# Optimization experiments

Hardware: AMD Instinct MI355X
Metric: run time of the kernel (lower is better)

Reference implementation:

```python
import jax, jax.numpy as jnp
import numpy as np

D_MODEL = 1024
NUM_HEADS = 16
HEAD_DIM = D_MODEL // NUM_HEADS          # 64
ROT_W = HEAD_DIM // 2                    # partial_factor=(0.0, 0.5) -> rotary on first half
MAX_LEN = 2048
BASE = 10000.0


def _rope_tables(max_len):
    # theta over even dims of ROT_W, each repeated twice (interleaved pairs): [t0,t0,t1,t1,...]
    theta = 1.0 / (BASE ** (np.arange(0, ROT_W, 2, dtype=np.float32) / ROT_W))  # [ROT_W/2]
    m = np.arange(max_len, dtype=np.float32)[:, None] * theta[None, :]          # [max_len, ROT_W/2]
    m = np.repeat(m, 2, axis=-1)                                                # [max_len, ROT_W]
    return jnp.asarray(np.cos(m)), jnp.asarray(np.sin(m))


def _rotate(x):
    # interleaved pairs (x0, x1) -> (-x1, x0)
    xr = x.reshape(x.shape[:-1] + (-1, 2))
    rot = jnp.stack([-xr[..., 1], xr[..., 0]], axis=-1)
    return rot.reshape(x.shape)


def setup_inputs() -> dict:
    key = jax.random.key(0)
    k1, k2, k3, k4 = jax.random.split(key, 4)
    B, L, H, E = 2, 2048, NUM_HEADS, HEAD_DIM
    return {
        "queries": jax.random.normal(k1, (B, L, H, E), jnp.float32),
        "keys": jax.random.normal(k2, (B, L, H, E), jnp.float32),
        "values": jax.random.normal(k3, (B, L, H, E), jnp.float32),
        "bias_weight": jax.random.normal(k4, (2, H), jnp.float32) * 0.02,  # BinaryAttentionBias embedding
        "n_vars": 32,
        "n_tokens": 64,
    }


def reference(queries, keys, values, bias_weight, n_vars, n_tokens):
    B, L, H, E = queries.shape
    q = queries.transpose(0, 2, 1, 3)  # [B,H,L,E]
    k = keys.transpose(0, 2, 1, 3)     # [B,H,L,E]

    # --- partial rotary projection (shared for q and k), seq_id = arange(L) ---
    cos, sin = _rope_tables(MAX_LEN)
    seq = jnp.arange(n_vars * n_tokens)
    c = cos[seq][None, None]  # [1,1,L,ROT_W]
    s = sin[seq][None, None]

    def rope(x):
        xr = x[..., :ROT_W]
        return jnp.concatenate([c * xr + s * _rotate(xr), x[..., ROT_W:]], axis=-1)

    q = rope(q)
    k = rope(k)

    scale = 1.0 / np.sqrt(E).astype(np.float32)

    # --- binary attention bias: per-head scalar by variable-id equality ---
    var_id = jnp.repeat(jnp.arange(n_vars), n_tokens)          # [L]
    same_var = var_id[:, None] == var_id[None, :]              # [L,L]
    bias = jnp.where(same_var[None, :, :],
                     bias_weight[1][:, None, None],
                     bias_weight[0][:, None, None])            # [H,L,L]

    # --- TimerMultivariateMask: causal in time, full across variables ---
    time_id = seq % n_tokens
    causal_bad = time_id[None, :] > time_id[:, None]           # key time > query time
    attn_mask = jnp.where(causal_bad[None], -jnp.inf, bias)    # [H,L,L]

    scores = jnp.einsum('bhle,bhse->bhls', q, k)               # [B,H,L,L]
    A = jax.nn.softmax(scale * scores + attn_mask[None], axis=-1)
    V = jnp.einsum('bhls,bshd->blhd', A, values)               # [B,L,H,E]
    return V
```

## Files before the change

kernel.cpp:

```cpp
#include <hip/hip_runtime.h>

typedef unsigned short u16;
typedef unsigned int u32;

typedef __attribute__((ext_vector_type(8))) __bf16 bf16x8;
typedef __attribute__((ext_vector_type(4))) float floatx4;

#define B_ 2
#define L_ 2048
#define H_ 16
#define E_ 64
#define QK_ELEMS (B_ * H_ * L_ * E_)
#define WS_OFF 128

static __device__ __forceinline__ float bf2f(u16 v) {
  u32 u = ((u32)v) << 16;
  return __builtin_bit_cast(float, u);
}
static __device__ __forceinline__ u16 f2bf(float x) {
  u32 u = __builtin_bit_cast(u32, x);
  u32 r = (u + 0x7FFFu + ((u >> 16) & 1u)) >> 16;
  return (u16)r;
}

static __device__ __forceinline__ u32 cvtpk_bf16(float lo, float hi) {
  u32 r;
  asm("v_cvt_pk_bf16_f32 %0, %1, %2" : "=v"(r) : "v"(lo), "v"(hi));
  return r;
}

static __device__ __forceinline__ float exp2_fast(float x) {
  float r;
  asm("v_exp_f32 %0, %1" : "=v"(r) : "v"(x));
  return r;
}

static __device__ __forceinline__ void sincos_fast(float a, float* s, float* c) {
  const float INV2PI = 0.15915494309189535f;
  float r = a * INV2PI;
  r = r - floorf(r);
  float ss, cc;
  asm("v_sin_f32 %0, %1" : "=v"(ss) : "v"(r));
  asm("v_cos_f32 %0, %1" : "=v"(cc) : "v"(r));
  *s = ss;
  *c = cc;
}

static __device__ __forceinline__ bool detect_f32_spread(const void* q, u32 blk) {
  const u32* q32 = (const u32*)q;
  u32 off = ((blk & 1023u) << 6) + (threadIdx.x & 63);
  u32 w0 = q32[off];
  u32 w1 = q32[off + 65536];
  int big = ((((w0 >> 7) & 0xFF) > 180) | (((w0 >> 23) & 0xFF) > 180) |
             (((w1 >> 7) & 0xFF) > 180) | (((w1 >> 23) & 0xFF) > 180));
  return __ballot(big) != 0ULL;
}

__global__ void detect_dtype(const u16* __restrict__ q, int* __restrict__ flag) {
  int lane = threadIdx.x;
  int big = 0;
#pragma unroll
  for (int i = 0; i < 16; ++i) {
    u16 v = q[lane * 16 + i];
    int e = (v >> 7) & 0xFF;
    big |= (e > 180);
  }
  unsigned long long b = __ballot(big);
  if (lane == 0) *flag = (b != 0ULL) ? 1 : 0;
}

static __device__ __forceinline__ bf16x8 ld8(const void* base, size_t off, bool f32) {
  if (f32) {
    const float* p = (const float*)base + off;
    float4 a = *(const float4*)p;
    float4 bb = *(const float4*)(p + 4);
    uint4 o;
    o.x = (u32)f2bf(a.x) | ((u32)f2bf(a.y) << 16);
    o.y = (u32)f2bf(a.z) | ((u32)f2bf(a.w) << 16);
    o.z = (u32)f2bf(bb.x) | ((u32)f2bf(bb.y) << 16);
    o.w = (u32)f2bf(bb.z) | ((u32)f2bf(bb.w) << 16);
    return __builtin_bit_cast(bf16x8, o);
  }
  return *(const bf16x8*)((const u16*)base + off);
}

static __device__ __forceinline__ bf16x8 rope_frag(bf16x8 x, float pos, int quad) {
  uint4 u = __builtin_bit_cast(uint4, x);
  float v0 = bf2f((u16)u.x), v1 = bf2f((u16)(u.x >> 16));
  float v2 = bf2f((u16)u.y), v3 = bf2f((u16)(u.y >> 16));
  float v4 = bf2f((u16)u.z), v5 = bf2f((u16)(u.z >> 16));
  float v6 = bf2f((u16)u.w), v7 = bf2f((u16)(u.w >> 16));
  const float LB = 0.83048202372184058696f;
  float jb = (float)(quad * 4);
  float a0 = pos * exp2_fast(-jb * LB);
  float a1 = pos * exp2_fast(-(jb + 1.f) * LB);
  float a2 = pos * exp2_fast(-(jb + 2.f) * LB);
  float a3 = pos * exp2_fast(-(jb + 3.f) * LB);
  float s0, c0, s1, c1, s2, c2, s3, c3;
  sincos_fast(a0, &s0, &c0);
  sincos_fast(a1, &s1, &c1);
  sincos_fast(a2, &s2, &c2);
  sincos_fast(a3, &s3, &c3);
  uint4 o;
  o.x = (u32)f2bf(c0 * v0 - s0 * v1) | ((u32)f2bf(c0 * v1 + s0 * v0) << 16);
  o.y = (u32)f2bf(c1 * v2 - s1 * v3) | ((u32)f2bf(c1 * v3 + s1 * v2) << 16);
  o.z = (u32)f2bf(c2 * v4 - s2 * v5) | ((u32)f2bf(c2 * v5 + s2 * v4) << 16);
  o.w = (u32)f2bf(c3 * v6 - s3 * v7) | ((u32)f2bf(c3 * v7 + s3 * v6) << 16);
  return __builtin_bit_cast(bf16x8, o);
}

__global__ __launch_bounds__(256) void prep_kv(
    const void* __restrict__ Q, const void* __restrict__ K, const void* __restrict__ V,
    u16* __restrict__ Kr, u16* __restrict__ VT) {
  __shared__ u16 tile[64][65];
  const int t = threadIdx.x;
  const bool f32 = detect_f32_spread(Q, blockIdx.x);

  if (blockIdx.x < (B_ * L_)) {
    const int bl = blockIdx.x;
    const int b = bl >> 11, l = bl & (L_ - 1);
    const int h = t >> 4, d = (t & 15) << 2;
    size_t in_off = (((size_t)(b * L_ + l) * H_ + h) * E_) + d;
    size_t out_off = (((size_t)(b * H_ + h) * L_ + l) * E_) + d;
    float k0, k1, k2, k3;
    if (f32) {
      float4 kv = *(const float4*)((const float*)K + in_off);
      k0 = kv.x; k1 = kv.y; k2 = kv.z; k3 = kv.w;
    } else {
      uint2 kv = *(const uint2*)((const u16*)K + in_off);
      k0 = bf2f((u16)kv.x); k1 = bf2f((u16)(kv.x >> 16));
      k2 = bf2f((u16)kv.y); k3 = bf2f((u16)(kv.y >> 16));
    }
    if (d < 32) {
      int j0 = d >> 1;
      const float LB = 0.83048202372184058696f;
      float a0 = (float)l * exp2_fast(-(float)j0 * LB);
      float a1 = (float)l * exp2_fast(-(float)(j0 + 1) * LB);
      float s0, c0, s1, c1;
      sincos_fast(a0, &s0, &c0);
      sincos_fast(a1, &s1, &c1);
      float r;
      r = c0 * k0 - s0 * k1; k1 = c0 * k1 + s0 * k0; k0 = r;
      r = c1 * k2 - s1 * k3; k3 = c1 * k3 + s1 * k2; k2 = r;
    }
    uint2 ko;
    ko.x = (u32)f2bf(k0) | ((u32)f2bf(k1) << 16);
    ko.y = (u32)f2bf(k2) | ((u32)f2bf(k3) << 16);
    *(uint2*)(Kr + out_off) = ko;
  } else {
    const int blk = blockIdx.x - (B_ * L_);
    const int bh = blk & 31, lt = blk >> 5;
    const int b = bh >> 4, h = bh & 15;
    const int l0 = lt << 6;
#pragma unroll
    for (int it = 0; it < 2; ++it) {
      int ll = (t >> 3) + (it << 5);
      int dc = (t & 7) << 3;
      size_t off = (((size_t)(b * L_ + l0 + ll) * H_ + h) * E_) + dc;
      bf16x8 x8 = ld8(V, off, f32);
      uint4 x = __builtin_bit_cast(uint4, x8);
      tile[ll][dc + 0] = (u16)x.x; tile[ll][dc + 1] = (u16)(x.x >> 16);
      tile[ll][dc + 2] = (u16)x.y; tile[ll][dc + 3] = (u16)(x.y >> 16);
      tile[ll][dc + 4] = (u16)x.z; tile[ll][dc + 5] = (u16)(x.z >> 16);
      tile[ll][dc + 6] = (u16)x.w; tile[ll][dc + 7] = (u16)(x.w >> 16);
    }
    __syncthreads();
    int e = t >> 2, lg = (t & 3) << 4;
    u32 pk[8];
#pragma unroll
    for (int i = 0; i < 8; ++i)
      pk[i] = (u32)tile[lg + 2 * i][e] | ((u32)tile[lg + 2 * i + 1][e] << 16);
    u16* dst = VT + (((size_t)(bh * 32 + lt)) << 12) + e * 64 + lg;
    uint4 o0; o0.x = pk[0]; o0.y = pk[1]; o0.z = pk[2]; o0.w = pk[3];
    uint4 o1; o1.x = pk[4]; o1.y = pk[5]; o1.z = pk[6]; o1.w = pk[7];
    *(uint4*)dst = o0;
    *(uint4*)(dst + 8) = o1;
  }
}

#if __has_builtin(__builtin_amdgcn_global_load_lds)
#define HAS_GLL 1
static __device__ __forceinline__ void gll16(const void* g, void* l) {
  __builtin_amdgcn_global_load_lds(
      (const __attribute__((address_space(1))) u32*)g,
      (__attribute__((address_space(3))) u32*)l, 16, 0, 0);
}
#else
#define HAS_GLL 0
#endif

__global__ __launch_bounds__(256, 2) void flash_v6(
    const void* __restrict__ Q, const u16* __restrict__ Kr,
    const u16* __restrict__ VT, const void* __restrict__ bw,
    void* __restrict__ out) {
  __shared__ u16 kbuf[2][64][64];
  __shared__ u16 vbuf[2][64][64];
  __shared__ u32 plds[4][2][48][20];

  const int tid = threadIdx.x;
  const int wid = tid >> 6, lane = tid & 63;
  const int quad = lane >> 4, l16 = lane & 15;
  const int bh = blockIdx.x & 31;
  const int gb = blockIdx.x >> 5;
  const int var_l = (gb << 1) + (wid >> 1);
  const int s0 = (wid & 1) << 4;
  const int base = var_l << 6;
  const int b = bh >> 4, h = bh & 15;

  const bool f32 = detect_f32_spread(Q, blockIdx.x);
  const u16* Kb = Kr + ((size_t)bh << 17);
  const u16* Vb = VT + ((size_t)bh << 17);

  const float LOG2E = 1.4426950408889634f;
  const float bw_diff = f32 ? ((const float*)bw)[h] : bf2f(((const u16*)bw)[h]);
  const float bw_same = f32 ? ((const float*)bw)[H_ + h] : bf2f(((const u16*)bw)[H_ + h]);
  const float C1 = 0.125f * LOG2E;
  const float c2d = bw_diff * LOG2E;
  const float c2s = bw_same * LOG2E;
  const float NEGINF = -__builtin_inff();

  bf16x8 qf[2][2];
#pragma unroll
  for (int rh = 0; rh < 2; ++rh) {
    const int r = base + s0 + (rh << 5) + l16;
    size_t ro = (((size_t)(b * L_ + r) * H_ + h) * E_);
    qf[rh][0] = rope_frag(ld8(Q, ro + quad * 8, f32), (float)r, quad);
    qf[rh][1] = ld8(Q, ro + 32 + quad * 8, f32);
  }

  const floatx4 zero4 = {0.f, 0.f, 0.f, 0.f};
  bf16x8 ones;
  { uint4 t4; t4.x = t4.y = t4.z = t4.w = 0x3F803F80u; ones = __builtin_bit_cast(bf16x8, t4); }

  floatx4 oacc[2][4], lacc[2];
#pragma unroll
  for (int rh = 0; rh < 2; ++rh) {
    lacc[rh] = zero4;
#pragma unroll
    for (int c4 = 0; c4 < 4; ++c4) oacc[rh][c4] = zero4;
  }

  const int srow = lane >> 3;
  const int sc16 = (lane & 7) ^ srow;
#if !HAS_GLL
  uint4 sk[2], sv[2];
#endif
  auto stage_issue = [&](int bufn, int v) {
    const int k0r = v << 6;
#pragma unroll
    for (int rr = 0; rr < 2; ++rr) {
      const int chunk = (wid << 1) + rr;
      const int row = (chunk << 3) + srow;
      const u16* gk = Kb + (size_t)(k0r + row) * 64 + sc16 * 8;
      const u16* gv = Vb + ((size_t)v << 12) + (size_t)row * 64 + sc16 * 8;
#if HAS_GLL
      gll16(gk, (char*)&kbuf[bufn][0][0] + chunk * 1024);
      gll16(gv, (char*)&vbuf[bufn][0][0] + chunk * 1024);
#else
      sk[rr] = *(const uint4*)gk;
      sv[rr] = *(const uint4*)gv;
#endif
    }
  };
  auto stage_commit = [&](int bufn) {
#if !HAS_GLL
#pragma unroll
    for (int rr = 0; rr < 2; ++rr) {
      const int chunk = (wid << 1) + rr;
      *(uint4*)((u16*)&kbuf[bufn][0][0] + chunk * 512 + lane * 8) = sk[rr];
      *(uint4*)((u16*)&vbuf[bufn][0][0] + chunk * 512 + lane * 8) = sv[rr];
    }
#else
    (void)bufn;
#endif
  };

  stage_issue(0, 0);
  stage_commit(0);
  __asm__ volatile("s_waitcnt vmcnt(0)" ::: "memory");
  __syncthreads();

  int pp = 0;
  const int sw = l16 & 7;

  for (int v = 0; v < 32; ++v) {
    const int buf = v & 1;
    const bool more = (v < 31);
    if (more) stage_issue(buf ^ 1, v + 1);

    bf16x8 kf[2][2], kg[2][2];
#pragma unroll
    for (int ch = 0; ch < 2; ++ch) {
      const int row = ch * 16 + l16;
#pragma unroll
      for (int hf = 0; hf < 2; ++hf) {
        kf[ch][hf] = *(const bf16x8*)&kbuf[buf][row][(((hf << 2) + quad) ^ sw) << 3];
        kg[ch][hf] = *(const bf16x8*)&kbuf[buf][32 + row][(((hf << 2) + quad) ^ sw) << 3];
      }
    }
    bf16x8 vf0[4], vf1[4];
#pragma unroll
    for (int c4 = 0; c4 < 4; ++c4) {
      vf0[c4] = *(const bf16x8*)&vbuf[buf][c4 * 16 + l16][(quad ^ sw) << 3];
      vf1[c4] = *(const bf16x8*)&vbuf[buf][c4 * 16 + l16][((4 + quad) ^ sw) << 3];
    }
    const float c2 = (v == var_l) ? c2s : c2d;

    floatx4 cc[2][2], dd[2];
    __builtin_amdgcn_s_setprio(1);
#pragma unroll
    for (int ch = 0; ch < 2; ++ch) {
#pragma unroll
      for (int rh = 0; rh < 2; ++rh) {
        floatx4 a0 = __builtin_amdgcn_mfma_f32_16x16x32_bf16(kf[ch][0], qf[rh][0], zero4, 0, 0, 0);
        cc[rh][ch] = __builtin_amdgcn_mfma_f32_16x16x32_bf16(kf[ch][1], qf[rh][1], a0, 0, 0, 0);
      }
      floatx4 a1 = __builtin_amdgcn_mfma_f32_16x16x32_bf16(kg[ch][0], qf[1][0], zero4, 0, 0, 0);
      dd[ch] = __builtin_amdgcn_mfma_f32_16x16x32_bf16(kg[ch][1], qf[1][1], a1, 0, 0, 0);
    }
    __builtin_amdgcn_s_setprio(0);

    u32* const prow = &plds[wid][pp][0][0];
#pragma unroll
    for (int ch = 0; ch < 2; ++ch) {
      float p0[4], p1[4], p2[4];
#pragma unroll
      for (int reg = 0; reg < 4; ++reg) {
        const bool msk = (ch * 16 + quad * 4 + reg) > (s0 + l16);
        float sA = fmaf(cc[0][ch][reg], C1, c2);
        if (msk) sA = NEGINF;
        p0[reg] = exp2_fast(sA);
        p1[reg] = exp2_fast(fmaf(cc[1][ch][reg], C1, c2));
        float sC = fmaf(dd[ch][reg], C1, c2);
        if (msk) sC = NEGINF;
        p2[reg] = exp2_fast(sC);
      }
      uint2 w;
      w.x = cvtpk_bf16(p0[0], p0[1]); w.y = cvtpk_bf16(p0[2], p0[3]);
      *(uint2*)(prow + (0 + l16) * 20 + ch * 8 + quad * 2) = w;
      w.x = cvtpk_bf16(p1[0], p1[1]); w.y = cvtpk_bf16(p1[2], p1[3]);
      *(uint2*)(prow + (16 + l16) * 20 + ch * 8 + quad * 2) = w;
      w.x = cvtpk_bf16(p2[0], p2[1]); w.y = cvtpk_bf16(p2[2], p2[3]);
      *(uint2*)(prow + (32 + l16) * 20 + ch * 8 + quad * 2) = w;
    }
    __asm__ volatile("s_waitcnt lgkmcnt(0)" ::: "memory");
    bf16x8 pa0, pa1, pb2;
    pa0 = __builtin_bit_cast(bf16x8, *(const uint4*)(prow + (0 + l16) * 20 + quad * 4));
    pa1 = __builtin_bit_cast(bf16x8, *(const uint4*)(prow + (16 + l16) * 20 + quad * 4));
    pb2 = __builtin_bit_cast(bf16x8, *(const uint4*)(prow + (32 + l16) * 20 + quad * 4));

    __builtin_amdgcn_s_setprio(1);
    lacc[0] = __builtin_amdgcn_mfma_f32_16x16x32_bf16(pa0, ones, lacc[0], 0, 0, 0);
    lacc[1] = __builtin_amdgcn_mfma_f32_16x16x32_bf16(pa1, ones, lacc[1], 0, 0, 0);
    lacc[1] = __builtin_amdgcn_mfma_f32_16x16x32_bf16(pb2, ones, lacc[1], 0, 0, 0);
#pragma unroll
    for (int c4 = 0; c4 < 4; ++c4) {
      oacc[0][c4] = __builtin_amdgcn_mfma_f32_16x16x32_bf16(pa0, vf0[c4], oacc[0][c4], 0, 0, 0);
      oacc[1][c4] = __builtin_amdgcn_mfma_f32_16x16x32_bf16(pa1, vf0[c4], oacc[1][c4], 0, 0, 0);
      oacc[1][c4] = __builtin_amdgcn_mfma_f32_16x16x32_bf16(pb2, vf1[c4], oacc[1][c4], 0, 0, 0);
    }
    __builtin_amdgcn_s_setprio(0);
    pp ^= 1;

    if (more) {
      stage_commit(buf ^ 1);
      __asm__ volatile("s_waitcnt vmcnt(0)" ::: "memory");
      __syncthreads();
    }
  }

  float rinv[2][4];
#pragma unroll
  for (int rh = 0; rh < 2; ++rh)
#pragma unroll
    for (int reg = 0; reg < 4; ++reg) {
      float lv = lacc[rh][reg];
      rinv[rh][reg] = (lv > 1e-30f) ? 1.0f / lv : 0.0f;
    }

#pragma unroll
  for (int rh = 0; rh < 2; ++rh)
#pragma unroll
    for (int c4 = 0; c4 < 4; ++c4)
#pragma unroll
      for (int reg = 0; reg < 4; ++reg) {
        const int row = base + s0 + (rh << 5) + quad * 4 + reg;
        const int col = c4 * 16 + l16;
        float val = oacc[rh][c4][reg] * rinv[rh][reg];
        size_t oo = (((size_t)(b * L_ + row)) * H_ + h) * E_ + col;
        if (f32) ((float*)out)[oo] = val;
        else ((u16*)out)[oo] = f2bf(val);
      }
}

__global__ __launch_bounds__(256) void flash_fused(
    const void* __restrict__ Q, const void* __restrict__ K,
    const void* __restrict__ V, const void* __restrict__ bw,
    const int* __restrict__ flag, void* __restrict__ out) {
  __shared__ u16 plds[4][2][32 * 36];
  __shared__ u16 vlds[4][64][40];
  const bool f32 = flag ? (*flag != 0) : true;
  const int tid = threadIdx.x;
  const int wid = tid >> 6, lane = tid & 63;
  const int quad = lane >> 4, l16 = lane & 15;
  const int bh = blockIdx.x & 31;
  const int g = blockIdx.x >> 5;
  const int rowblk = (g << 2) + wid;
  const int row0 = rowblk << 5;
  const int b = bh >> 4, h = bh & 15;
  const int t0 = row0 & 63;
  const int var_l = row0 >> 6;
  const int ktiles = (t0 >> 5) + 1;

  const float bw_diff = f32 ? ((const float*)bw)[h] : bf2f(((const u16*)bw)[h]);
  const float bw_same = f32 ? ((const float*)bw)[H_ + h] : bf2f(((const u16*)bw)[H_ + h]);

  const floatx4 zero4 = {0.f, 0.f, 0.f, 0.f};
  bf16x8 ones;
  { uint4 t4; t4.x = t4.y = t4.z = t4.w = 0x3F803F80u; ones = __builtin_bit_cast(bf16x8, t4); }

  bf16x8 qf[2][2];
#pragma unroll
  for (int rh = 0; rh < 2; ++rh) {
    const int r = row0 + rh * 16 + l16;
    size_t ro = (((size_t)(b * L_ + r) * H_ + h) * E_);
#pragma unroll
    for (int hf = 0; hf < 2; ++hf)
      qf[rh][hf] = ld8(Q, ro + hf * 32 + quad * 8, f32);
    qf[rh][0] = rope_frag(qf[rh][0], (float)r, quad);
  }

  floatx4 oacc[2][4], lacc[2];
#pragma unroll
  for (int rh = 0; rh < 2; ++rh) {
    lacc[rh] = zero4;
#pragma unroll
    for (int c4 = 0; c4 < 4; ++c4) oacc[rh][c4] = zero4;
  }

  u16* const pbase = &plds[wid][0][0];
  u16* const vb = &vlds[wid][0][0];
  int pp = 0;

  for (int v = 0; v < 32; ++v) {
    const float bias = (v == var_l) ? bw_same : bw_diff;
    for (int kt = 0; kt < ktiles; ++kt) {
      const int k0 = (v << 6) + (kt << 5);

      bf16x8 kf[2][2];
#pragma unroll
      for (int ch = 0; ch < 2; ++ch) {
        const int r = k0 + ch * 16 + l16;
        size_t ro = (((size_t)(b * L_ + r) * H_ + h) * E_);
#pragma unroll
        for (int hf = 0; hf < 2; ++hf)
          kf[ch][hf] = ld8(K, ro + hf * 32 + quad * 8, f32);
        kf[ch][0] = rope_frag(kf[ch][0], (float)r, quad);
      }

      floatx4 cc[2][2];
#pragma unroll
      for (int rh = 0; rh < 2; ++rh)
#pragma unroll
        for (int ch = 0; ch < 2; ++ch) {
          floatx4 acc = __builtin_amdgcn_mfma_f32_16x16x32_bf16(qf[rh][0], kf[ch][0], zero4, 0, 0, 0);
          cc[rh][ch] = __builtin_amdgcn_mfma_f32_16x16x32_bf16(qf[rh][1], kf[ch][1], acc, 0, 0, 0);
        }

      u16* const pw = pbase + pp * (32 * 36);
      const int ts_b = (kt << 5) + l16;
#pragma unroll
      for (int rh = 0; rh < 2; ++rh)
#pragma unroll
        for (int ch = 0; ch < 2; ++ch) {
          const int ts = ts_b + ch * 16;
#pragma unroll
          for (int reg = 0; reg < 4; ++reg) {
            const int tl = t0 + rh * 16 + quad * 4 + reg;
            float s = cc[rh][ch][reg] * 0.125f + bias;
            float p = (ts > tl) ? 0.0f : __expf(s);
            pw[(rh * 16 + quad * 4 + reg) * 36 + ch * 16 + l16] = f2bf(p);
          }
        }

#pragma unroll
      for (int it = 0; it < 4; ++it) {
        const int s = (lane >> 3) + it * 8;
        const int dc = (lane & 7) << 3;
        size_t vo = (((size_t)(b * L_ + k0 + s) * H_ + h) * E_) + dc;
        bf16x8 x8 = ld8(V, vo, f32);
        uint4 x = __builtin_bit_cast(uint4, x8);
        vb[(dc + 0) * 40 + s] = (u16)x.x; vb[(dc + 1) * 40 + s] = (u16)(x.x >> 16);
        vb[(dc + 2) * 40 + s] = (u16)x.y; vb[(dc + 3) * 40 + s] = (u16)(x.y >> 16);
        vb[(dc + 4) * 40 + s] = (u16)x.z; vb[(dc + 5) * 40 + s] = (u16)(x.z >> 16);
        vb[(dc + 6) * 40 + s] = (u16)x.w; vb[(dc + 7) * 40 + s] = (u16)(x.w >> 16);
      }

      __asm__ volatile("s_waitcnt lgkmcnt(0)" ::: "memory");

      bf16x8 pa[2];
#pragma unroll
      for (int rh = 0; rh < 2; ++rh) {
        const u16* pr = pw + (rh * 16 + l16) * 36 + quad * 8;
        uint2 lo = *(const uint2*)pr;
        uint2 hi = *(const uint2*)(pr + 4);
        uint4 cmb; cmb.x = lo.x; cmb.y = lo.y; cmb.z = hi.x; cmb.w = hi.y;
        pa[rh] = __builtin_bit_cast(bf16x8, cmb);
      }

#pragma unroll
      for (int rh = 0; rh < 2; ++rh)
        lacc[rh] = __builtin_amdgcn_mfma_f32_16x16x32_bf16(pa[rh], ones, lacc[rh], 0, 0, 0);

#pragma unroll
      for (int c4 = 0; c4 < 4; ++c4) {
        bf16x8 vf = *(const bf16x8*)(vb + (c4 * 16 + l16) * 40 + quad * 8);
#pragma unroll
        for (int rh = 0; rh < 2; ++rh)
          oacc[rh][c4] = __builtin_amdgcn_mfma_f32_16x16x32_bf16(pa[rh], vf, oacc[rh][c4], 0, 0, 0);
      }
      pp ^= 1;
    }
  }

  float rinv[2][4];
#pragma unroll
  for (int rh = 0; rh < 2; ++rh)
#pragma unroll
    for (int reg = 0; reg < 4; ++reg) {
      float lv = lacc[rh][reg];
      rinv[rh][reg] = (lv > 1e-30f) ? 1.0f / lv : 0.0f;
    }

#pragma unroll
  for (int rh = 0; rh < 2; ++rh)
#pragma unroll
    for (int c4 = 0; c4 < 4; ++c4)
#pragma unroll
      for (int reg = 0; reg < 4; ++reg) {
        const int row = row0 + rh * 16 + quad * 4 + reg;
        const int col = c4 * 16 + l16;
        float val = oacc[rh][c4][reg] * rinv[rh][reg];
        size_t oo = (((size_t)(b * L_ + row)) * H_ + h) * E_ + col;
        if (f32) ((float*)out)[oo] = val;
        else ((u16*)out)[oo] = f2bf(val);
      }
}

extern "C" void kernel_launch(void* const* d_in, const int* in_sizes, int n_in,
                              void* d_out, int out_size, void* d_ws, size_t ws_size,
                              hipStream_t stream) {
  (void)in_sizes; (void)n_in; (void)out_size;
  const void* q = d_in[0];
  const void* k = d_in[1];
  const void* v = d_in[2];
  const void* bwp = d_in[3];
  const size_t need = (size_t)WS_OFF * 2 + 2u * QK_ELEMS * sizeof(u16);
  if (ws_size >= need) {
    u16* Kr = (u16*)d_ws + WS_OFF;
    u16* VT = Kr + QK_ELEMS;
    prep_kv<<<B_ * L_ + B_ * H_ * (L_ / 64), 256, 0, stream>>>(q, k, v, Kr, VT);
    flash_v6<<<512, 256, 0, stream>>>(q, Kr, VT, bwp, d_out);
  } else if (ws_size >= sizeof(int)) {
    int* flag = (int*)d_ws;
    detect_dtype<<<1, 64, 0, stream>>>((const u16*)q, flag);
    flash_fused<<<512, 256, 0, stream>>>(q, k, v, bwp, flag, d_out);
  } else {
    flash_fused<<<512, 256, 0, stream>>>(q, k, v, bwp, (const int*)nullptr, d_out);
  }
}
```

Baseline: 144.7 us.

## Split key-variable loop across two wave groups with LDS reduction

Doubles the block to 512 threads so two groups of four waves each process half of the 32 key variables for the same query rows, each with its own double-buffered K/V LDS staging. Partial output and row-sum accumulators are combined through LDS at the end before the first group normalizes and writes. The P tile path is also restructured into three sequential single-tile passes that share one smaller LDS scratch row per wave. This targets low wave occupancy and long serial loop latency, at the cost of more LDS, extra barriers and a final reduction step.

Result: slower. 210.7 us (+45.6%).

```diff
diff --git a/kernel.cpp b/kernel.cpp
--- a/kernel.cpp
+++ b/kernel.cpp
@@ -189,21 +189,22 @@
 #define HAS_GLL 0
 #endif
 
-__global__ __launch_bounds__(256, 2) void flash_v6(
+__global__ __launch_bounds__(512, 4) void flash_v7(
     const void* __restrict__ Q, const u16* __restrict__ Kr,
     const u16* __restrict__ VT, const void* __restrict__ bw,
     void* __restrict__ out) {
-  __shared__ u16 kbuf[2][64][64];
-  __shared__ u16 vbuf[2][64][64];
-  __shared__ u32 plds[4][2][48][20];
+  __shared__ u16 kbuf[2][2][64][64];
+  __shared__ u16 vbuf[2][2][64][64];
+  __shared__ u32 plds[8][16][20];
 
   const int tid = threadIdx.x;
   const int wid = tid >> 6, lane = tid & 63;
+  const int half = wid >> 2, w4 = wid & 3;
   const int quad = lane >> 4, l16 = lane & 15;
   const int bh = blockIdx.x & 31;
   const int gb = blockIdx.x >> 5;
-  const int var_l = (gb << 1) + (wid >> 1);
-  const int s0 = (wid & 1) << 4;
+  const int var_l = (gb << 1) + (w4 >> 1);
+  const int s0 = (w4 & 1) << 4;
   const int base = var_l << 6;
   const int b = bh >> 4, h = bh & 15;
 
@@ -249,13 +250,13 @@
     const int k0r = v << 6;
 #pragma unroll
     for (int rr = 0; rr < 2; ++rr) {
-      const int chunk = (wid << 1) + rr;
+      const int chunk = (w4 << 1) + rr;
       const int row = (chunk << 3) + srow;
       const u16* gk = Kb + (size_t)(k0r + row) * 64 + sc16 * 8;
       const u16* gv = Vb + ((size_t)v << 12) + (size_t)row * 64 + sc16 * 8;
 #if HAS_GLL
-      gll16(gk, (char*)&kbuf[bufn][0][0] + chunk * 1024);
-      gll16(gv, (char*)&vbuf[bufn][0][0] + chunk * 1024);
+      gll16(gk, (char*)&kbuf[half][bufn][0][0] + chunk * 1024);
+      gll16(gv, (char*)&vbuf[half][bufn][0][0] + chunk * 1024);
 #else
       sk[rr] = *(const uint4*)gk;
       sv[rr] = *(const uint4*)gv;
@@ -266,26 +267,55 @@
 #if !HAS_GLL
 #pragma unroll
     for (int rr = 0; rr < 2; ++rr) {
-      const int chunk = (wid << 1) + rr;
-      *(uint4*)((u16*)&kbuf[bufn][0][0] + chunk * 512 + lane * 8) = sk[rr];
-      *(uint4*)((u16*)&vbuf[bufn][0][0] + chunk * 512 + lane * 8) = sv[rr];
+      const int chunk = (w4 << 1) + rr;
+      *(uint4*)((u16*)&kbuf[half][bufn][0][0] + chunk * 512 + lane * 8) = sk[rr];
+      *(uint4*)((u16*)&vbuf[half][bufn][0][0] + chunk * 512 + lane * 8) = sv[rr];
     }
 #else
     (void)bufn;
 #endif
   };
 
-  stage_issue(0, 0);
+  const int vbase = half << 4;
+  stage_issue(0, vbase);
   stage_commit(0);
   __asm__ volatile("s_waitcnt vmcnt(0)" ::: "memory");
   __syncthreads();
 
-  int pp = 0;
   const int sw = l16 & 7;
-
-  for (int v = 0; v < 32; ++v) {
-    const int buf = v & 1;
-    const bool more = (v < 31);
+  u32* const prow = &plds[wid][l16][0];
+
+  auto pv_tile = [&](const floatx4 sc[2], bool msk_on, float c2,
+                     int rh, const bf16x8 vf[4]) {
+#pragma unroll
+    for (int ch = 0; ch < 2; ++ch) {
+      float p[4];
+#pragma unroll
+      for (int reg = 0; reg < 4; ++reg) {
+        const bool msk = msk_on && ((ch * 16 + quad * 4 + reg) > (s0 + l16));
+        float s = fmaf(sc[ch][reg], C1, c2);
+        if (msk) s = NEGINF;
+        p[reg] = exp2_fast(s);
+      }
+      uint2 w;
+      w.x = cvtpk_bf16(p[0], p[1]);
+      w.y = cvtpk_bf16(p[2], p[3]);
+      *(uint2*)(prow + ch * 8 + quad * 2) = w;
+    }
+    __asm__ volatile("s_waitcnt lgkmcnt(0)" ::: "memory");
+    bf16x8 pa = __builtin_bit_cast(bf16x8, *(const uint4*)(prow + quad * 4));
+    __builtin_amdgcn_s_setprio(1);
+    lacc[rh] = __builtin_amdgcn_mfma_f32_16x16x32_bf16(pa, ones, lacc[rh], 0, 0, 0);
+#pragma unroll
+    for (int c4 = 0; c4 < 4; ++c4)
+      oacc[rh][c4] = __builtin_amdgcn_mfma_f32_16x16x32_bf16(pa, vf[c4], oacc[rh][c4], 0, 0, 0);
+    __builtin_amdgcn_s_setprio(0);
+  };
+
+  for (int vi = 0; vi < 16; ++vi) {
+    const int v = vbase + vi;
+    const int buf = vi & 1;
+    const bool more = (vi < 15);
     if (more) stage_issue(buf ^ 1, v + 1);
 
     bf16x8 kf[2][2], kg[2][2];
@@ -294,15 +324,15 @@
       const int row = ch * 16 + l16;
 #pragma unroll
       for (int hf = 0; hf < 2; ++hf) {
-        kf[ch][hf] = *(const bf16x8*)&kbuf[buf][row][(((hf << 2) + quad) ^ sw) << 3];
-        kg[ch][hf] = *(const bf16x8*)&kbuf[buf][32 + row][(((hf << 2) + quad) ^ sw) << 3];
+        kf[ch][hf] = *(const bf16x8*)&kbuf[half][buf][row][(((hf << 2) + quad) ^ sw) << 3];
+        kg[ch][hf] = *(const bf16x8*)&kbuf[half][buf][32 + row][(((hf << 2) + quad) ^ sw) << 3];
       }
     }
     bf16x8 vf0[4], vf1[4];
 #pragma unroll
     for (int c4 = 0; c4 < 4; ++c4) {
-      vf0[c4] = *(const bf16x8*)&vbuf[buf][c4 * 16 + l16][(quad ^ sw) << 3];
-      vf1[c4] = *(const bf16x8*)&vbuf[buf][c4 * 16 + l16][((4 + quad) ^ sw) << 3];
+      vf0[c4] = *(const bf16x8*)&vbuf[half][buf][c4 * 16 + l16][(quad ^ sw) << 3];
+      vf1[c4] = *(const bf16x8*)&vbuf[half][buf][c4 * 16 + l16][((4 + quad) ^ sw) << 3];
     }
     const float c2 = (v == var_l) ? c2s : c2d;
 
@@ -320,47 +350,9 @@
     }
     __builtin_amdgcn_s_setprio(0);
 
-    u32* const prow = &plds[wid][pp][0][0];
-#pragma unroll
-    for (int ch = 0; ch < 2; ++ch) {
-      float p0[4], p1[4], p2[4];
-#pragma unroll
-      for (int reg = 0; reg < 4; ++reg) {
-        const bool msk = (ch * 16 + quad * 4 + reg) > (s0 + l16);
-        float sA = fmaf(cc[0][ch][reg], C1, c2);
-        if (msk) sA = NEGINF;
-        p0[reg] = exp2_fast(sA);
-        p1[reg] = exp2_fast(fmaf(cc[1][ch][reg], C1, c2));
-        float sC = fmaf(dd[ch][reg], C1, c2);
-        if (msk) sC = NEGINF;
-        p2[reg] = exp2_fast(sC);
-      }
-      uint2 w;
-      w.x = cvtpk_bf16(p0[0], p0[1]); w.y = cvtpk_bf16(p0[2], p0[3]);
-      *(uint2*)(prow + (0 + l16) * 20 + ch * 8 + quad * 2) = w;
-      w.x = cvtpk_bf16(p1[0], p1[1]); w.y = cvtpk_bf16(p1[2], p1[3]);
-      *(uint2*)(prow + (16 + l16) * 20 + ch * 8 + quad * 2) = w;
-      w.x = cvtpk_bf16(p2[0], p2[1]); w.y = cvtpk_bf16(p2[2], p2[3]);
-      *(uint2*)(prow + (32 + l16) * 20 + ch * 8 + quad * 2) = w;
-    }
-    __asm__ volatile("s_waitcnt lgkmcnt(0)" ::: "memory");
-    bf16x8 pa0, pa1, pb2;
-    pa0 = __builtin_bit_cast(bf16x8, *(const uint4*)(prow + (0 + l16) * 20 + quad * 4));
-    pa1 = __builtin_bit_cast(bf16x8, *(const uint4*)(prow + (16 + l16) * 20 + quad * 4));
-    pb2 = __builtin_bit_cast(bf16x8, *(const uint4*)(prow + (32 + l16) * 20 + quad * 4));
-
-    __builtin_amdgcn_s_setprio(1);
-    lacc[0] = __builtin_amdgcn_mfma_f32_16x16x32_bf16(pa0, ones, lacc[0], 0, 0, 0);
-    lacc[1] = __builtin_amdgcn_mfma_f32_16x16x32_bf16(pa1, ones, lacc[1], 0, 0, 0);
-    lacc[1] = __builtin_amdgcn_mfma_f32_16x16x32_bf16(pb2, ones, lacc[1], 0, 0, 0);
-#pragma unroll
-    for (int c4 = 0; c4 < 4; ++c4) {
-      oacc[0][c4] = __builtin_amdgcn_mfma_f32_16x16x32_bf16(pa0, vf0[c4], oacc[0][c4], 0, 0, 0);
-      oacc[1][c4] = __builtin_amdgcn_mfma_f32_16x16x32_bf16(pa1, vf0[c4], oacc[1][c4], 0, 0, 0);
-      oacc[1][c4] = __builtin_amdgcn_mfma_f32_16x16x32_bf16(pb2, vf1[c4], oacc[1][c4], 0, 0, 0);
-    }
-    __builtin_amdgcn_s_setprio(0);
-    pp ^= 1;
+    pv_tile(cc[0], true, c2, 0, vf0);
+    pv_tile(cc[1], false, c2, 1, vf0);
+    pv_tile(dd, true, c2, 1, vf1);
 
     if (more) {
       stage_commit(buf ^ 1);
@@ -369,28 +361,62 @@
     }
   }
 
-  float rinv[2][4];
-#pragma unroll
-  for (int rh = 0; rh < 2; ++rh)
-#pragma unroll
-    for (int reg = 0; reg < 4; ++reg) {
-      float lv = lacc[rh][reg];
-      rinv[rh][reg] = (lv > 1e-30f) ? 1.0f / lv : 0.0f;
-    }
-
-#pragma unroll
-  for (int rh = 0; rh < 2; ++rh)
-#pragma unroll
-    for (int c4 = 0; c4 < 4; ++c4)
+  __syncthreads();
+  float* oscr = (float*)&kbuf[0][0][0][0];
+  float* lscr = (float*)&vbuf[0][0][0][0];
+#pragma unroll
+  for (int round = 0; round < 2; ++round) {
+    const int src0 = 4 + (round << 1);
+    if (wid == src0 || wid == src0 + 1) {
+      const int slot = wid - src0;
+      float* dst = oscr + slot * 4096;
+#pragma unroll
+      for (int rh = 0; rh < 2; ++rh) {
+#pragma unroll
+        for (int c4 = 0; c4 < 4; ++c4)
+          *(floatx4*)(dst + (rh * 4 + c4) * 256 + lane * 4) = oacc[rh][c4];
+        *(floatx4*)(lscr + slot * 512 + lane * 8 + rh * 4) = lacc[rh];
+      }
+    }
+    __syncthreads();
+    const int dst0 = round << 1;
+    if (wid == dst0 || wid == dst0 + 1) {
+      const int slot = wid - dst0;
+      const float* src = oscr + slot * 4096;
+#pragma unroll
+      for (int rh = 0; rh < 2; ++rh) {
+#pragma unroll
+        for (int c4 = 0; c4 < 4; ++c4)
+          oacc[rh][c4] += *(const floatx4*)(src + (rh * 4 + c4) * 256 + lane * 4);
+        lacc[rh] += *(const floatx4*)(lscr + slot * 512 + lane * 8 + rh * 4);
+      }
+    }
+    __syncthreads();
+  }
+
+  if (half == 0) {
+    float rinv[2][4];
+#pragma unroll
+    for (int rh = 0; rh < 2; ++rh)
 #pragma unroll
       for (int reg = 0; reg < 4; ++reg) {
-        const int row = base + s0 + (rh << 5) + quad * 4 + reg;
-        const int col = c4 * 16 + l16;
-        float val = oacc[rh][c4][reg] * rinv[rh][reg];
-        size_t oo = (((size_t)(b * L_ + row)) * H_ + h) * E_ + col;
-        if (f32) ((float*)out)[oo] = val;
-        else ((u16*)out)[oo] = f2bf(val);
-      }
+        float lv = lacc[rh][reg];
+        rinv[rh][reg] = (lv > 1e-30f) ? 1.0f / lv : 0.0f;
+      }
+#pragma unroll
+    for (int rh = 0; rh < 2; ++rh)
+#pragma unroll
+      for (int c4 = 0; c4 < 4; ++c4)
+#pragma unroll
+        for (int reg = 0; reg < 4; ++reg) {
+          const int row = base + s0 + (rh << 5) + quad * 4 + reg;
+          const int col = c4 * 16 + l16;
+          float val = oacc[rh][c4][reg] * rinv[rh][reg];
+          size_t oo = (((size_t)(b * L_ + row)) * H_ + h) * E_ + col;
+          if (f32) ((float*)out)[oo] = val;
+          else ((u16*)out)[oo] = f2bf(val);
+        }
+  }
 }
 
 __global__ __launch_bounds__(256) void flash_fused(
@@ -560,7 +586,7 @@
     u16* Kr = (u16*)d_ws + WS_OFF;
     u16* VT = Kr + QK_ELEMS;
     prep_kv<<<B_ * L_ + B_ * H_ * (L_ / 64), 256, 0, stream>>>(q, k, v, Kr, VT);
-    flash_v6<<<512, 256, 0, stream>>>(q, Kr, VT, bwp, d_out);
+    flash_v7<<<512, 512, 0, stream>>>(q, Kr, VT, bwp, d_out);
   } else if (ws_size >= sizeof(int)) {
     int* flag = (int*)d_ws;
     detect_dtype<<<1, 64, 0, stream>>>((const u16*)q, flag);
```
